# Performance work log

Measured on AMD Instinct MI355X. Metric: run time of the kernel, lower is better.

Reference implementation:

```python
import jax, jax.numpy as jnp
import numpy as np


def setup_inputs() -> dict:
    key = jax.random.key(0)
    B, C, T = 16, 128, 8192
    x = jax.random.normal(key, (B, C, T), dtype=jnp.float32)
    return {"x": x}


def reference(x) -> jnp.ndarray:
    # x: (B, C, T) real EEG signals
    B, C, T = x.shape
    # "Analytic" signal as in the torch code: zero FFT bins >= T//2, then ifft.
    Xf = jnp.fft.fft(x, axis=-1)                       # complex64 (B, C, T)
    keep = (jnp.arange(T) < (T // 2))                  # (T,)
    Xf = jnp.where(keep, Xf, 0.0 + 0.0j)
    xa = jnp.fft.ifft(Xf, axis=-1)                     # complex analytic signal
    phase = jnp.arctan2(xa.imag, xa.real)              # == torch.angle, (B, C, T)

    # PLV_ij = |mean_t exp(i(phase_i - phase_j))|
    # Decompose: Re = mean(cos_i cos_j + sin_i sin_j), Im = mean(sin_i cos_j - cos_i sin_j)
    cos_p = jnp.cos(phase)                             # (B, C, T)
    sin_p = jnp.sin(phase)
    inv_t = jnp.float32(1.0 / T)
    re = (jnp.einsum('bct,bdt->bcd', cos_p, cos_p)
          + jnp.einsum('bct,bdt->bcd', sin_p, sin_p)) * inv_t
    im = (jnp.einsum('bct,bdt->bcd', sin_p, cos_p)
          - jnp.einsum('bct,bdt->bcd', cos_p, sin_p)) * inv_t
    plv = jnp.sqrt(re * re + im * im)                  # (B, C, C)
    return plv
```

## Files before the change

### kernel.cpp

```cpp
#include <hip/hip_runtime.h>
#include <hip/hip_fp16.h>
#include <math.h>

#define T_LEN 8192
#define CHN 128
#define BATCH 16
#define NKCHUNK 32
#define KSTAGE 64
#define NITER (T_LEN / NKCHUNK / KSTAGE)

typedef short bf16x8 __attribute__((ext_vector_type(8)));
typedef float f32x16 __attribute__((ext_vector_type(16)));

#define SIN8 0.3826834323650898f
#define COS8 0.9238795325112868f
#define SROW 72
#define SPLANE (128 * SROW)

__device__ __forceinline__ ushort f2bf(float f) {
    unsigned u = __float_as_uint(f);
    unsigned r = (u + 0x7fffu + ((u >> 16) & 1u)) >> 16;
    return (ushort)r;
}

__device__ __forceinline__ void barrier_lds_only() {
    asm volatile("s_waitcnt lgkmcnt(0)" ::: "memory");
    __builtin_amdgcn_s_barrier();
}

__device__ __forceinline__ float2 cadd(float2 a, float2 b) { return make_float2(a.x + b.x, a.y + b.y); }
__device__ __forceinline__ float2 csub(float2 a, float2 b) { return make_float2(a.x - b.x, a.y - b.y); }
__device__ __forceinline__ float2 cmul(float2 a, float2 b) {
    return make_float2(a.x * b.x - a.y * b.y, a.x * b.y + a.y * b.x);
}

__device__ __forceinline__ void r4f(float2 x0, float2 x1, float2 x2, float2 x3,
                                    float2 wa, float2 wb, float2 wc,
                                    float2& y0, float2& y1, float2& y2, float2& y3) {
    float2 t0 = cadd(x0, x2), t1 = csub(x0, x2);
    float2 t2 = cadd(x1, x3), t3 = csub(x1, x3);
    y0 = cadd(t0, t2);
    y1 = cmul(csub(t0, t2), wb);
    y2 = cmul(make_float2(t1.x + t3.y, t1.y - t3.x), wa);
    y3 = cmul(make_float2(t1.x - t3.y, t1.y + t3.x), wc);
}

__device__ __forceinline__ void r4i(float2 x0, float2 x1, float2 x2, float2 x3,
                                    float2 wa, float2 wb, float2 wc,
                                    float2& y0, float2& y1, float2& y2, float2& y3) {
    float2 a1 = cmul(x1, wb);
    float2 a2 = cmul(x2, wa);
    float2 a3 = cmul(x3, wc);
    float2 u0 = cadd(x0, a1), u1 = csub(x0, a1);
    float2 p = cadd(a2, a3);
    float2 m = make_float2(-(a2.y - a3.y), a2.x - a3.x);
    y0 = cadd(u0, p); y2 = csub(u0, p);
    y1 = cadd(u1, m); y3 = csub(u1, m);
}

__device__ __forceinline__ void r8f(const float2* x, float sn, float cs, float2* y) {
    const float r22 = 0.70710678118654752f;
    float2 w1 = make_float2(cs, sn);
    float2 w2 = make_float2(cs * cs - sn * sn, 2.f * cs * sn);
    float2 w4 = cmul(w2, w2);
    float2 w6 = cmul(w4, w2);
    float2 u0 = cadd(x[0], x[4]), u1 = cadd(x[1], x[5]), u2 = cadd(x[2], x[6]), u3 = cadd(x[3], x[7]);
    float2 e0 = cmul(csub(x[0], x[4]), w1);
    float2 e1 = cmul(csub(x[1], x[5]), w1);
    float2 e2 = cmul(csub(x[2], x[6]), w1);
    float2 e3 = cmul(csub(x[3], x[7]), w1);
    float2 v0 = e0;
    float2 v1 = make_float2(r22 * (e1.x + e1.y), r22 * (e1.y - e1.x));
    float2 v2 = make_float2(e2.y, -e2.x);
    float2 v3 = make_float2(r22 * (e3.y - e3.x), -r22 * (e3.x + e3.y));
    r4f(u0, u1, u2, u3, w2, w4, w6, y[0], y[1], y[2], y[3]);
    r4f(v0, v1, v2, v3, w2, w4, w6, y[4], y[5], y[6], y[7]);
}

__device__ __forceinline__ void r8i(const float2* x, float sn, float cs, float2* y) {
    const float r22 = 0.70710678118654752f;
    float2 w1 = make_float2(cs, sn);
    float2 w2 = make_float2(cs * cs - sn * sn, 2.f * cs * sn);
    float2 w4 = cmul(w2, w2);
    float2 w6 = cmul(w4, w2);
    float2 g0, g1, g2, g3, g4, g5, g6, g7;
    r4i(x[0], x[1], x[2], x[3], w2, w4, w6, g0, g1, g2, g3);
    r4i(x[4], x[5], x[6], x[7], w2, w4, w6, g4, g5, g6, g7);
    float2 t0 = cmul(g4, w1);
    float2 e1 = cmul(g5, w1);
    float2 e2 = cmul(g6, w1);
    float2 e3 = cmul(g7, w1);
    float2 t1 = make_float2(r22 * (e1.x - e1.y), r22 * (e1.x + e1.y));
    float2 t2 = make_float2(-e2.y, e2.x);
    float2 t3 = make_float2(-r22 * (e3.x + e3.y), r22 * (e3.x - e3.y));
    y[0] = cadd(g0, t0); y[4] = csub(g0, t0);
    y[1] = cadd(g1, t1); y[5] = csub(g1, t1);
    y[2] = cadd(g2, t2); y[6] = csub(g2, t2);
    y[3] = cadd(g3, t3); y[7] = csub(g3, t3);
}

__global__ __launch_bounds__(512, 4) void fft_analytic_kernel(const float* __restrict__ x,
                                                              ushort* __restrict__ zc,
                                                              ushort* __restrict__ zs) {
    __shared__ __align__(16) float2 buf[T_LEN];
    const int tid = threadIdx.x;
    const int row = blockIdx.x;
    const float* xr = x + ((size_t)row << 13);

    for (int s = 0; s < 2; ++s) {
        const int g = tid + (s << 9);
        float2 X[8], Y[8];
#pragma unroll
        for (int c = 0; c < 8; ++c) X[c] = make_float2(xr[g + (c << 10)], 0.f);
        float sn, cs;
        __sincosf(-(float)M_PI / 4096.f * (float)g, &sn, &cs);
        r8f(X, sn, cs, Y);
#pragma unroll
        for (int c = 0; c < 8; ++c) buf[g + (c << 10)] = Y[c];
    }
    __syncthreads();

    {
        const float astep = -(float)M_PI / 512.f;
        for (int s = 0; s < 2; ++s) {
            const int g = tid + (s << 9);
            const int j = g & 127;
            const int i = ((g & ~127) << 3) | j;
            float2 xx[8], yy[8];
#pragma unroll
            for (int c = 0; c < 8; ++c) xx[c] = buf[i + c * 128];
            float sn, cs;
            __sincosf(astep * (float)j, &sn, &cs);
            r8f(xx, sn, cs, yy);
#pragma unroll
            for (int c = 0; c < 8; ++c) buf[i + c * 128] = yy[c];
        }
        __syncthreads();
    }

    {
        const float astep = -(float)M_PI / 64.f;
        for (int s = 0; s < 2; ++s) {
            const int g = tid + (s << 9);
            const int j = g & 15;
            const int i = ((g & ~15) << 3) | j;
            float2 xx[8], yy[8];
#pragma unroll
            for (int c = 0; c < 8; ++c) xx[c] = buf[i + c * 16];
            float sn, cs;
            __sincosf(astep * (float)j, &sn, &cs);
            r8f(xx, sn, cs, yy);
#pragma unroll
            for (int c = 0; c < 8; ++c) buf[(i + c * 16) ^ (2 * c)] = yy[c];
        }
        __syncthreads();
    }

    {
        float2 v[16];
        float4* bb = (float4*)buf;
        const int K = tid & 7;
#pragma unroll
        for (int p = 0; p < 8; ++p) {
            float4 f = bb[8 * tid + (p ^ K)];
            v[2 * p]     = make_float2(f.x, f.y);
            v[2 * p + 1] = make_float2(f.z, f.w);
        }
        float2 xe[8], xo[8], E[8], O[8], t[8];
#pragma unroll
        for (int c = 0; c < 8; ++c) { xe[c] = v[2 * c]; xo[c] = v[2 * c + 1]; }
        r8f(xe, 0.f, 1.f, E);
        r8f(xo, -SIN8, COS8, O);
#pragma unroll
        for (int c = 0; c < 8; ++c) t[c] = cadd(E[c], O[c]);
        r8i(t, 0.f, 1.f, xe);
        r8i(t, SIN8, COS8, xo);
#pragma unroll
        for (int p = 0; p < 8; ++p)
            bb[8 * tid + (p ^ K)] = make_float4(xe[p].x, xe[p].y, xo[p].x, xo[p].y);
    }
    __syncthreads();

    {
        const float astep = (float)M_PI / 64.f;
        for (int s = 0; s < 2; ++s) {
            const int g = tid + (s << 9);
            const int j = g & 15;
            const int i = ((g & ~15) << 3) | j;
            float2 xx[8], yy[8];
#pragma unroll
            for (int c = 0; c < 8; ++c) xx[c] = buf[(i + c * 16) ^ (2 * c)];
            float sn, cs;
            __sincosf(astep * (float)j, &sn, &cs);
            r8i(xx, sn, cs, yy);
#pragma unroll
            for (int c = 0; c < 8; ++c) buf[i + c * 16] = yy[c];
        }
        __syncthreads();
    }

    {
        const float astep = (float)M_PI / 512.f;
        for (int s = 0; s < 2; ++s) {
            const int g = tid + (s << 9);
            const int j = g & 127;
            const int i = ((g & ~127) << 3) | j;
            float2 xx[8], yy[8];
#pragma unroll
            for (int c = 0; c < 8; ++c) xx[c] = buf[i + c * 128];
            float sn, cs;
            __sincosf(astep * (float)j, &sn, &cs);
            r8i(xx, sn, cs, yy);
#pragma unroll
            for (int c = 0; c < 8; ++c) buf[i + c * 128] = yy[c];
        }
        __syncthreads();
    }

    ushort* zcr = zc + ((size_t)row << 13);
    ushort* zsr = zs + ((size_t)row << 13);
    for (int s = 0; s < 2; ++s) {
        const int g = tid + (s << 9);
        float2 xx[8], yy[8];
#pragma unroll
        for (int c = 0; c < 8; ++c) xx[c] = buf[g + (c << 10)];
        float sn, cs;
        __sincosf((float)M_PI / 4096.f * (float)g, &sn, &cs);
        r8i(xx, sn, cs, yy);
#pragma unroll
        for (int c = 0; c < 8; ++c) {
            float2 vv = yy[c];
            float n2 = vv.x * vv.x + vv.y * vv.y;
            float cc = 1.f, ss = 0.f;
            if (n2 > 0.f) { float inv = rsqrtf(n2); cc = vv.x * inv; ss = vv.y * inv; }
            zcr[g + (c << 10)] = f2bf(cc);
            zsr[g + (c << 10)] = f2bf(ss);
        }
    }
}

__global__ __launch_bounds__(512, 2) void gram_kernel(const ushort* __restrict__ zc,
                                                      const ushort* __restrict__ zs,
                                                      __half2* __restrict__ partial) {
    const int b = blockIdx.x, kc = blockIdx.y;
    const int tid = threadIdx.x;
    const int wave = tid >> 6;
    const int wr = wave & 3, wcol = wave >> 2;
    const int lane31 = tid & 31;
    const int half = (tid >> 5) & 1;

    __shared__ __align__(16) ushort sZ[2 * SPLANE];

    f32x16 accRe[2], accIm[2];
#pragma unroll
    for (int v = 0; v < 2; ++v)
#pragma unroll
        for (int r = 0; r < 16; ++r) { accRe[v][r] = 0.f; accIm[v][r] = 0.f; }

    const size_t base = ((size_t)b * CHN) << 13;
    const int k0 = kc << 8;

    const ushort* srcs[4];
    int ldst[4];
#pragma unroll
    for (int q = 0; q < 4; ++q) {
        int id = tid + (q << 9);
        int plane = id >> 10;
        int rid = (id >> 3) & 127;
        int ck = id & 7;
        srcs[q] = (plane ? zs : zc) + base + ((size_t)rid << 13) + (size_t)(k0 + ck * 8);
        ldst[q] = plane * SPLANE + rid * SROW + ck * 8;
    }

    uint4 pre[2][4];
#pragma unroll
    for (int q = 0; q < 4; ++q) pre[0][q] = *(const uint4*)srcs[q];
#pragma unroll
    for (int q = 0; q < 4; ++q) pre[1][q] = *(const uint4*)(srcs[q] + KSTAGE);

#pragma unroll
    for (int it = 0; it < NITER; ++it) {
        barrier_lds_only();
#pragma unroll
        for (int q = 0; q < 4; ++q) *(uint4*)&sZ[ldst[q]] = pre[it & 1][q];
        if (it < NITER - 2) {
#pragma unroll
            for (int q = 0; q < 4; ++q)
                pre[it & 1][q] = *(const uint4*)(srcs[q] + (it + 2) * KSTAGE);
        }
        barrier_lds_only();
#pragma unroll
        for (int kb = 0; kb < KSTAGE; kb += 16) {
            const int aoff = (wr * 32 + lane31) * SROW + kb + half * 8;
            bf16x8 aC = *(const bf16x8*)&sZ[aoff];
            bf16x8 aS = *(const bf16x8*)&sZ[SPLANE + aoff];
            bf16x8 aCn;
#pragma unroll
            for (int r = 0; r < 8; ++r) aCn[r] = (short)(aC[r] ^ (short)0x8000);
            bf16x8 bC[2], bS[2];
#pragma unroll
            for (int v = 0; v < 2; ++v) {
                const int boff = (wcol * 64 + v * 32 + lane31) * SROW + kb + half * 8;
                bC[v] = *(const bf16x8*)&sZ[boff];
                bS[v] = *(const bf16x8*)&sZ[SPLANE + boff];
            }
            accRe[0] = __builtin_amdgcn_mfma_f32_32x32x16_bf16(aC,  bC[0], accRe[0], 0, 0, 0);
            accRe[1] = __builtin_amdgcn_mfma_f32_32x32x16_bf16(aC,  bC[1], accRe[1], 0, 0, 0);
            accIm[0] = __builtin_amdgcn_mfma_f32_32x32x16_bf16(aS,  bC[0], accIm[0], 0, 0, 0);
            accIm[1] = __builtin_amdgcn_mfma_f32_32x32x16_bf16(aS,  bC[1], accIm[1], 0, 0, 0);
            accRe[0] = __builtin_amdgcn_mfma_f32_32x32x16_bf16(aS,  bS[0], accRe[0], 0, 0, 0);
            accRe[1] = __builtin_amdgcn_mfma_f32_32x32x16_bf16(aS,  bS[1], accRe[1], 0, 0, 0);
            accIm[0] = __builtin_amdgcn_mfma_f32_32x32x16_bf16(aCn, bS[0], accIm[0], 0, 0, 0);
            accIm[1] = __builtin_amdgcn_mfma_f32_32x32x16_bf16(aCn, bS[1], accIm[1], 0, 0, 0);
        }
    }

    __half2* pb = partial + ((size_t)(kc * BATCH + b) << 14);
#pragma unroll
    for (int v = 0; v < 2; ++v)
#pragma unroll
        for (int r = 0; r < 16; ++r) {
            int rrow = (r & 3) + 8 * (r >> 2) + 4 * half;
            int i = wr * 32 + rrow;
            int j = wcol * 64 + v * 32 + lane31;
            pb[i * CHN + j] = __floats2half2_rn(accRe[v][r], accIm[v][r]);
        }
}

__global__ __launch_bounds__(256) void reduce_kernel(const __half2* __restrict__ partial,
                                                     float* __restrict__ out) {
    const size_t i = (size_t)blockIdx.x * 256 + threadIdx.x;
    const size_t n = (size_t)BATCH * CHN * CHN;
    if (i >= n) return;
    float re = 0.0f, im = 0.0f;
#pragma unroll
    for (int c = 0; c < NKCHUNK; ++c) {
        float2 p = __half22float2(partial[(size_t)c * n + i]);
        re += p.x;
        im += p.y;
    }
    out[i] = sqrtf(re * re + im * im) * (1.0f / (float)T_LEN);
}

extern "C" void kernel_launch(void* const* d_in, const int* in_sizes, int n_in,
                              void* d_out, int out_size, void* d_ws, size_t ws_size,
                              hipStream_t stream) {
    const float* x = (const float*)d_in[0];
    float* out = (float*)d_out;

    const size_t plane_elems = (size_t)BATCH * CHN * T_LEN;
    ushort* zc = (ushort*)d_ws;
    ushort* zs = zc + plane_elems;
    __half2* partial = (__half2*)((char*)d_ws + 2 * plane_elems * sizeof(ushort));

    fft_analytic_kernel<<<BATCH * CHN, 512, 0, stream>>>(x, zc, zs);

    dim3 g2(BATCH, NKCHUNK);
    gram_kernel<<<g2, 512, 0, stream>>>(zc, zs, partial);

    const int n_out = BATCH * CHN * CHN;
    reduce_kernel<<<(n_out + 255) / 256, 256, 0, stream>>>(partial, out);
}
```

Before: 184.6 us.

## Stream gram tiles with direct global-to-LDS loads into swizzled double buffers

Replaces the register-staged global loads plus LDS stores in the gram kernel with global_load_lds direct transfers into two LDS buffers, waited on with vmcnt. The padded row stride is replaced by an XOR swizzle of 16-byte chunks, which keeps LDS reads conflict-free without padding. The aim is to free VGPRs and VALU store work so the launch-bound occupancy hint can be raised from 2 to 4 blocks. The cost is a larger LDS footprint from double buffering and a dependence on correct vmcnt accounting and the swizzle mapping.

```diff
diff --git a/kernel.cpp b/kernel.cpp
--- a/kernel.cpp
+++ b/kernel.cpp
@@ -14,8 +14,13 @@
 
 #define SIN8 0.3826834323650898f
 #define COS8 0.9238795325112868f
-#define SROW 72
-#define SPLANE (128 * SROW)
+
+#define KROW 64
+#define SPLANE (128 * KROW)
+#define BUFSZ (2 * SPLANE)
+
+typedef const __attribute__((address_space(1))) uint gld_src_t;
+typedef __attribute__((address_space(3))) uint gld_dst_t;
 
 __device__ __forceinline__ ushort f2bf(float f) {
     unsigned u = __float_as_uint(f);
@@ -239,17 +244,18 @@
     }
 }
 
-__global__ __launch_bounds__(512, 2) void gram_kernel(const ushort* __restrict__ zc,
+__global__ __launch_bounds__(512, 4) void gram_kernel(const ushort* __restrict__ zc,
                                                       const ushort* __restrict__ zs,
                                                       __half2* __restrict__ partial) {
     const int b = blockIdx.x, kc = blockIdx.y;
     const int tid = threadIdx.x;
     const int wave = tid >> 6;
+    const int lane = tid & 63;
     const int wr = wave & 3, wcol = wave >> 2;
     const int lane31 = tid & 31;
     const int half = (tid >> 5) & 1;
 
-    __shared__ __align__(16) ushort sZ[2 * SPLANE];
+    __shared__ __align__(16) ushort sZ[2 * BUFSZ];
 
     f32x16 accRe[2], accIm[2];
 #pragma unroll
@@ -260,49 +266,55 @@
     const size_t base = ((size_t)b * CHN) << 13;
     const int k0 = kc << 8;
 
-    const ushort* srcs[4];
-    int ldst[4];
+    const ushort* gsrc[4];
+    int lbase[4];
 #pragma unroll
     for (int q = 0; q < 4; ++q) {
-        int id = tid + (q << 9);
-        int plane = id >> 10;
-        int rid = (id >> 3) & 127;
-        int ck = id & 7;
-        srcs[q] = (plane ? zs : zc) + base + ((size_t)rid << 13) + (size_t)(k0 + ck * 8);
-        ldst[q] = plane * SPLANE + rid * SROW + ck * 8;
-    }
-
-    uint4 pre[2][4];
-#pragma unroll
-    for (int q = 0; q < 4; ++q) pre[0][q] = *(const uint4*)srcs[q];
-#pragma unroll
-    for (int q = 0; q < 4; ++q) pre[1][q] = *(const uint4*)(srcs[q] + KSTAGE);
+        int L = (q * 8 + wave) * 64 + lane;
+        int plane = L >> 10;
+        int r = (L >> 3) & 127;
+        int slot = L & 7;
+        int c = slot ^ (r & 7);
+        gsrc[q] = (plane ? zs : zc) + base + ((size_t)r << 13) + (size_t)(k0 + c * 8);
+        lbase[q] = (q * 8 + wave) * 512;
+    }
+
+#define STAGE(IT, BUF) do {                                                        \
+        _Pragma("unroll")                                                          \
+        for (int q = 0; q < 4; ++q)                                                \
+            __builtin_amdgcn_global_load_lds(                                      \
+                (gld_src_t*)(gsrc[q] + (IT) * KSTAGE),                             \
+                (gld_dst_t*)&sZ[(BUF) * BUFSZ + lbase[q]], 16, 0, 0);              \
+    } while (0)
+
+    STAGE(0, 0);
+    STAGE(1, 1);
 
 #pragma unroll
     for (int it = 0; it < NITER; ++it) {
-        barrier_lds_only();
-#pragma unroll
-        for (int q = 0; q < 4; ++q) *(uint4*)&sZ[ldst[q]] = pre[it & 1][q];
-        if (it < NITER - 2) {
-#pragma unroll
-            for (int q = 0; q < 4; ++q)
-                pre[it & 1][q] = *(const uint4*)(srcs[q] + (it + 2) * KSTAGE);
-        }
-        barrier_lds_only();
+        if (it < NITER - 1) { asm volatile("s_waitcnt vmcnt(4)" ::: "memory"); }
+        else                { asm volatile("s_waitcnt vmcnt(0)" ::: "memory"); }
+        __builtin_amdgcn_sched_barrier(0);
+        __builtin_amdgcn_s_barrier();
+
+        const ushort* S = sZ + (it & 1) * BUFSZ;
 #pragma unroll
         for (int kb = 0; kb < KSTAGE; kb += 16) {
-            const int aoff = (wr * 32 + lane31) * SROW + kb + half * 8;
-            bf16x8 aC = *(const bf16x8*)&sZ[aoff];
-            bf16x8 aS = *(const bf16x8*)&sZ[SPLANE + aoff];
+            const int cA = (kb >> 3) + half;
+            const int rowA = wr * 32 + lane31;
+            const int aoff = rowA * KROW + ((cA ^ (rowA & 7)) << 3);
+            bf16x8 aC = *(const bf16x8*)&S[aoff];
+            bf16x8 aS = *(const bf16x8*)&S[SPLANE + aoff];
             bf16x8 aCn;
 #pragma unroll
             for (int r = 0; r < 8; ++r) aCn[r] = (short)(aC[r] ^ (short)0x8000);
             bf16x8 bC[2], bS[2];
 #pragma unroll
             for (int v = 0; v < 2; ++v) {
-                const int boff = (wcol * 64 + v * 32 + lane31) * SROW + kb + half * 8;
-                bC[v] = *(const bf16x8*)&sZ[boff];
-                bS[v] = *(const bf16x8*)&sZ[SPLANE + boff];
+                const int rowB = wcol * 64 + v * 32 + lane31;
+                const int boff = rowB * KROW + ((cA ^ (rowB & 7)) << 3);
+                bC[v] = *(const bf16x8*)&S[boff];
+                bS[v] = *(const bf16x8*)&S[SPLANE + boff];
             }
             accRe[0] = __builtin_amdgcn_mfma_f32_32x32x16_bf16(aC,  bC[0], accRe[0], 0, 0, 0);
             accRe[1] = __builtin_amdgcn_mfma_f32_32x32x16_bf16(aC,  bC[1], accRe[1], 0, 0, 0);
@@ -313,7 +325,11 @@
             accIm[0] = __builtin_amdgcn_mfma_f32_32x32x16_bf16(aCn, bS[0], accIm[0], 0, 0, 0);
             accIm[1] = __builtin_amdgcn_mfma_f32_32x32x16_bf16(aCn, bS[1], accIm[1], 0, 0, 0);
         }
-    }
+
+        barrier_lds_only();
+        if (it + 2 < NITER) STAGE(it + 2, it & 1);
+    }
+#undef STAGE
 
     __half2* pb = partial + ((size_t)(kc * BATCH + b) << 14);
 #pragma unroll
```

Measured after the change: 176.5 us. -4.4%, faster.
